# Optimization experiments

Measured on AMD Instinct MI355X. Metric: run time of the kernel, lower is better.

The kernel has to match this reference:

```python
import jax, jax.numpy as jnp
import numpy as np

LC, LQ, BATCH, D = 1024, 512, 64, 256

def setup_inputs() -> dict:
    key = jax.random.key(0)
    k1, k2, k3, k4, k5 = jax.random.split(key, 5)
    return {
        "C": jax.random.normal(k1, (LC, BATCH, D), dtype=jnp.float32),
        "Q": jax.random.normal(k2, (LQ, BATCH, D), dtype=jnp.float32),
        "w4C": jax.random.normal(k3, (D, 1), dtype=jnp.float32) * 0.05,
        "w4Q": jax.random.normal(k4, (D, 1), dtype=jnp.float32) * 0.05,
        "w4mlu": jax.random.normal(k5, (1, 1, D), dtype=jnp.float32) * 0.05,
        "bias": jnp.zeros((1,), dtype=jnp.float32),
    }

def reference(C, Q, w4C, w4Q, w4mlu, bias):
    # seq-major -> batch-major: (L, B, D) -> (B, L, D)
    C = jnp.transpose(C, (1, 0, 2))  # (B, Lc, D)
    Q = jnp.transpose(Q, (1, 0, 2))  # (B, Lq, D)
    # trilinear attention scores (dropout is identity in eval mode)
    sub0 = C @ w4C                                      # (B, Lc, 1)
    sub1 = jnp.transpose(Q @ w4Q, (0, 2, 1))            # (B, 1, Lq)
    sub2 = jnp.einsum('bcd,bqd->bcq', C * w4mlu, Q)     # (B, Lc, Lq)
    S = sub0 + sub1 + sub2 + bias                       # (B, Lc, Lq)
    S1 = jax.nn.softmax(S, axis=2)   # row softmax over query positions
    S2 = jax.nn.softmax(S, axis=1)   # col softmax over context positions
    A = jnp.einsum('bcq,bqd->bcd', S1, Q)               # (B, Lc, D)
    B_ = jnp.einsum('bck,bqk->bcq', S1, S2)             # S1 @ S2^T : (B, Lc, Lc)
    B_ = jnp.einsum('bce,bed->bcd', B_, C)              # (B, Lc, D)
    out = jnp.concatenate([C, A, C * A, C * B_], axis=2)  # (B, Lc, 4D)
    return jnp.transpose(out, (0, 2, 1))                  # (B, 4D, Lc)
```

## Files before the change

kernel.cpp:

```cpp
#include <hip/hip_runtime.h>

#define LCc 1024
#define LQq 512
#define BB  64
#define DDim 256

typedef __attribute__((ext_vector_type(8))) short bf16x8;
typedef __attribute__((ext_vector_type(4))) float f32x4;
typedef __attribute__((ext_vector_type(4))) unsigned short us4;
typedef __attribute__((ext_vector_type(8))) unsigned short us8;

static __device__ __forceinline__ unsigned short f2b(float f) {
  unsigned u = __builtin_bit_cast(unsigned, f);
  unsigned r = u + 0x7FFFu + ((u >> 16) & 1u);
  return (unsigned short)(r >> 16);
}
static __device__ __forceinline__ bf16x8 ldb8(const unsigned short* p) {
  return *(const bf16x8*)p;
}
static __device__ __forceinline__ f32x4 MFMA16(bf16x8 a, bf16x8 b, f32x4 c) {
  return __builtin_amdgcn_mfma_f32_16x16x32_bf16(a, b, c, 0, 0, 0);
}
static __device__ __forceinline__ void gload16(const unsigned short* g, unsigned short* l) {
  __builtin_amdgcn_global_load_lds(
      (const __attribute__((address_space(1))) unsigned int*)g,
      (__attribute__((address_space(3))) unsigned int*)l, 16, 0, 0);
}

__global__ __launch_bounds__(256, 4) void prep_CF(const float* __restrict__ C,
    const float* __restrict__ w4C, const float* __restrict__ w4mlu,
    unsigned short* __restrict__ Cw, unsigned short* __restrict__ CT,
    float* __restrict__ rowAdd) {
  __shared__ unsigned short tile[64][65];
  int c0 = blockIdx.x * 64, b = blockIdx.y;
  int t = threadIdx.x, r = t >> 2, g = t & 3;
  float rsum = 0.f;
  for (int dch = 0; dch < 4; dch++) {
    int d0 = dch * 64;
    const float* src = C + ((size_t)(c0 + r) * BB + b) * DDim + d0 + g * 16;
    unsigned short cwv[16];
    #pragma unroll
    for (int i = 0; i < 4; i++) {
      float4 v = ((const float4*)src)[i];
      float4 wm = *(const float4*)(w4mlu + d0 + g * 16 + i * 4);
      float4 wc = *(const float4*)(w4C + d0 + g * 16 + i * 4);
      rsum += v.x * wc.x + v.y * wc.y + v.z * wc.z + v.w * wc.w;
      cwv[i * 4 + 0] = f2b(v.x * wm.x);
      cwv[i * 4 + 1] = f2b(v.y * wm.y);
      cwv[i * 4 + 2] = f2b(v.z * wm.z);
      cwv[i * 4 + 3] = f2b(v.w * wm.w);
      tile[r][g * 16 + i * 4 + 0] = f2b(v.x);
      tile[r][g * 16 + i * 4 + 1] = f2b(v.y);
      tile[r][g * 16 + i * 4 + 2] = f2b(v.z);
      tile[r][g * 16 + i * 4 + 3] = f2b(v.w);
    }
    unsigned short* cwp = Cw + ((size_t)((b << 10) + c0 + r)) * DDim + d0 + g * 16;
    *(us8*)cwp = *(us8*)&cwv[0];
    *(us8*)(cwp + 8) = *(us8*)&cwv[8];
    __syncthreads();
    unsigned short* ctp = CT + ((size_t)((b << 8) + d0 + r)) * LCc + c0 + g * 16;
    us8 o0, o1;
    #pragma unroll
    for (int j = 0; j < 8; j++) { o0[j] = tile[g * 16 + j][r]; o1[j] = tile[g * 16 + 8 + j][r]; }
    *(us8*)ctp = o0;
    *(us8*)(ctp + 8) = o1;
    __syncthreads();
  }
  rsum += __shfl_xor(rsum, 1);
  rsum += __shfl_xor(rsum, 2);
  if (g == 0) rowAdd[((size_t)b << 10) + c0 + r] = rsum;
}

__global__ __launch_bounds__(256, 4) void prep_QF(const float* __restrict__ Q,
    const float* __restrict__ w4Q, const float* __restrict__ bias,
    unsigned short* __restrict__ Qb, unsigned short* __restrict__ QT,
    float* __restrict__ colAdd, float* __restrict__ colL) {
  __shared__ unsigned short tile[64][65];
  int q0 = blockIdx.x * 64, b = blockIdx.y;
  int t = threadIdx.x, r = t >> 2, g = t & 3;
  float rsum = 0.f;
  for (int dch = 0; dch < 4; dch++) {
    int d0 = dch * 64;
    const float* src = Q + ((size_t)(q0 + r) * BB + b) * DDim + d0 + g * 16;
    #pragma unroll
    for (int i = 0; i < 4; i++) {
      float4 v = ((const float4*)src)[i];
      float4 wq = *(const float4*)(w4Q + d0 + g * 16 + i * 4);
      rsum += v.x * wq.x + v.y * wq.y + v.z * wq.z + v.w * wq.w;
      tile[r][g * 16 + i * 4 + 0] = f2b(v.x);
      tile[r][g * 16 + i * 4 + 1] = f2b(v.y);
      tile[r][g * 16 + i * 4 + 2] = f2b(v.z);
      tile[r][g * 16 + i * 4 + 3] = f2b(v.w);
    }
    __syncthreads();
    unsigned short* qbp = Qb + ((size_t)((b << 9) + q0 + r)) * DDim + d0 + g * 16;
    us8 s0, s1;
    #pragma unroll
    for (int j = 0; j < 8; j++) { s0[j] = tile[r][g * 16 + j]; s1[j] = tile[r][g * 16 + 8 + j]; }
    *(us8*)qbp = s0;
    *(us8*)(qbp + 8) = s1;
    unsigned short* qtp = QT + ((size_t)((b << 8) + d0 + r)) * LQq + q0 + g * 16;
    us8 o0, o1;
    #pragma unroll
    for (int j = 0; j < 8; j++) { o0[j] = tile[g * 16 + j][r]; o1[j] = tile[g * 16 + 8 + j][r]; }
    *(us8*)qtp = o0;
    *(us8*)(qtp + 8) = o1;
    __syncthreads();
  }
  rsum += __shfl_xor(rsum, 1);
  rsum += __shfl_xor(rsum, 2);
  if (g == 0) {
    colAdd[((size_t)b << 9) + q0 + r] = rsum + bias[0];
    colL[((size_t)b << 9) + q0 + r] = 0.0f;
  }
}

__global__ __launch_bounds__(256, 3) void k_P(const unsigned short* __restrict__ Cw,
    const unsigned short* __restrict__ Qb, const float* __restrict__ rowAdd,
    const float* __restrict__ colAdd, unsigned short* __restrict__ Pt,
    float* __restrict__ rowL, float* __restrict__ colL) {
  int blk = blockIdx.x;
  int b = blk >> 4, ct = blk & 15;
  int t = threadIdx.x, w = t >> 6, lane = t & 63;
  int col = lane & 15, quad = lane >> 4;
  int c0w = ct * 64 + w * 16;
  __shared__ unsigned short tile[2][64][40];
  __shared__ float colAcc[LQq];
  for (int i = t; i < LQq; i += 256) colAcc[i] = 0.f;
  __syncthreads();

  bf16x8 afrag[8];
  const unsigned short* aPtr = Cw + ((size_t)((b << 10) + c0w + col)) * DDim + quad * 8;
  #pragma unroll
  for (int kk = 0; kk < 8; kk++) afrag[kk] = ldb8(aPtr + kk * 32);
  float rAddv[4];
  #pragma unroll
  for (int r = 0; r < 4; r++) rAddv[r] = rowAdd[((size_t)b << 10) + c0w + quad * 4 + r];
  float rowSum[4] = {0.f, 0.f, 0.f, 0.f};

  int cur = 0;
  for (int win = 0; win < 16; win++) {
    #pragma unroll
    for (int h = 0; h < 2; h++) {
      int q0 = win * 32 + h * 16;
      const unsigned short* bPtr = Qb + ((size_t)((b << 9) + q0 + col)) * DDim + quad * 8;
      f32x4 acc = {0.f, 0.f, 0.f, 0.f};
      #pragma unroll
      for (int kk = 0; kk < 8; kk++) acc = MFMA16(afrag[kk], ldb8(bPtr + kk * 32), acc);
      float cAdd = colAdd[((size_t)b << 9) + q0 + col];
      float csum = 0.f;
      #pragma unroll
      for (int r = 0; r < 4; r++) {
        float e = __expf(acc[r] + rAddv[r] + cAdd);
        rowSum[r] += e;
        csum += e;
        tile[cur][w * 16 + quad * 4 + r][h * 16 + col] = f2b(e);
      }
      csum += __shfl_xor(csum, 16);
      csum += __shfl_xor(csum, 32);
      if (lane < 16) atomicAdd(&colAcc[q0 + lane], csum);
    }
    __syncthreads();
    us8 frag = *(const us8*)&tile[cur][w * 16 + col][quad * 8];
    *(us8*)(Pt + (((size_t)(b * 64 + ct * 4 + w) * 16 + win) << 9) + lane * 8) = frag;
    cur ^= 1;
  }
  #pragma unroll
  for (int r = 0; r < 4; r++) {
    float s = rowSum[r];
    s += __shfl_xor(s, 1); s += __shfl_xor(s, 2);
    s += __shfl_xor(s, 4); s += __shfl_xor(s, 8);
    if (col == 0) rowL[((size_t)b << 10) + c0w + quad * 4 + r] = s;
  }
  __syncthreads();
  for (int i = t; i < LQq; i += 256) atomicAdd(&colL[((size_t)b << 9) + i], colAcc[i]);
}

__global__ __launch_bounds__(256, 4) void k_T(const unsigned short* __restrict__ Pt,
    const unsigned short* __restrict__ CT, const float* __restrict__ colL,
    unsigned short* __restrict__ TT) {
  int blk = blockIdx.x;
  int b = blk >> 4, qs = blk & 15;
  int t = threadIdx.x, w = t >> 6, lane = t & 63;
  int col = lane & 15, quad = lane >> 4;
  int dq = w * 64;
  int cbl = w & 1, jh = w >> 1;
  __shared__ unsigned short pT[32][40];

  f32x4 accT[2][4];
  #pragma unroll
  for (int mf = 0; mf < 2; mf++)
    #pragma unroll
    for (int nf = 0; nf < 4; nf++) accT[mf][nf] = (f32x4){0.f, 0.f, 0.f, 0.f};

  us8 frag = *(const us8*)(Pt + (((size_t)(b * 64 + 0 * 2 + cbl) * 16 + qs) << 9) + lane * 8);
  for (int cs = 0; cs < 32; cs++) {
    bf16x8 bf[4];
    #pragma unroll
    for (int nf = 0; nf < 4; nf++)
      bf[nf] = ldb8(CT + ((size_t)((b << 8) + dq + nf * 16 + col)) * LCc + cs * 32 + quad * 8);
    #pragma unroll
    for (int jj = 0; jj < 4; jj++) {
      int j = jh * 4 + jj;
      pT[quad * 8 + j][cbl * 16 + col] = (unsigned short)frag[j];
    }
    __syncthreads();
    bf16x8 pa[2];
    #pragma unroll
    for (int mf = 0; mf < 2; mf++) pa[mf] = *(const bf16x8*)&pT[mf * 16 + col][quad * 8];
    #pragma unroll
    for (int mf = 0; mf < 2; mf++)
      #pragma unroll
      for (int nf = 0; nf < 4; nf++) accT[mf][nf] = MFMA16(pa[mf], bf[nf], accT[mf][nf]);
    if (cs < 31)
      frag = *(const us8*)(Pt + (((size_t)(b * 64 + (cs + 1) * 2 + cbl) * 16 + qs) << 9) + lane * 8);
    __syncthreads();
  }
  float cInv[2][4];
  #pragma unroll
  for (int mf = 0; mf < 2; mf++)
    #pragma unroll
    for (int r = 0; r < 4; r++)
      cInv[mf][r] = 1.0f / colL[((size_t)b << 9) + qs * 32 + mf * 16 + quad * 4 + r];
  #pragma unroll
  for (int mf = 0; mf < 2; mf++)
    #pragma unroll
    for (int nf = 0; nf < 4; nf++) {
      us4 ov;
      #pragma unroll
      for (int r = 0; r < 4; r++) ov[r] = f2b(accT[mf][nf][r] * cInv[mf][r]);
      *(us4*)(TT + ((size_t)((b << 8) + dq + nf * 16 + col)) * LQq + qs * 32 + mf * 16 + quad * 4) = ov;
    }
}

__global__ __launch_bounds__(256, 2) void k_AB(const unsigned short* __restrict__ Pt,
    const unsigned short* __restrict__ QT, const unsigned short* __restrict__ TT,
    const float* __restrict__ rowL, const float* __restrict__ C,
    float* __restrict__ out) {
  int blk = blockIdx.x;
  int b = blk >> 4, ct = blk & 15;
  int t = threadIdx.x, w = t >> 6, lane = t & 63;
  int col = lane & 15, quad = lane >> 4;
  int dq = w * 64;
  __shared__ unsigned short sb[4][2][8][512];

  f32x4 accA[4][4], accB[4][4];
  #pragma unroll
  for (int mf = 0; mf < 4; mf++)
    #pragma unroll
    for (int nf = 0; nf < 4; nf++) {
      accA[mf][nf] = (f32x4){0.f, 0.f, 0.f, 0.f};
      accB[mf][nf] = (f32x4){0.f, 0.f, 0.f, 0.f};
    }

  #define STAGE(qs_, buf_)                                                              \
    {                                                                                   \
      int _q = (qs_) * 32 + quad * 8;                                                   \
      _Pragma("unroll")                                                                 \
      for (int nf = 0; nf < 4; nf++) {                                                  \
        size_t rowD = (size_t)((b << 8) + dq + nf * 16 + col);                          \
        gload16(QT + (rowD << 9) + _q, &sb[w][buf_][nf][0]);                            \
        gload16(TT + (rowD << 9) + _q, &sb[w][buf_][4 + nf][0]);                        \
      }                                                                                 \
    }

  bf16x8 pa[4], paN[4];
  #pragma unroll
  for (int mf = 0; mf < 4; mf++)
    pa[mf] = ldb8(Pt + (((size_t)(b * 64 + ct * 4 + mf) * 16 + 0) << 9) + lane * 8);
  STAGE(0, 0);
  __syncthreads();

  for (int qs = 0; qs < 16; qs++) {
    int bufr = qs & 1;
    if (qs < 15) {
      STAGE(qs + 1, bufr ^ 1);
      #pragma unroll
      for (int mf = 0; mf < 4; mf++)
        paN[mf] = ldb8(Pt + (((size_t)(b * 64 + ct * 4 + mf) * 16 + qs + 1) << 9) + lane * 8);
    }
    bf16x8 bq[4], bt[4];
    #pragma unroll
    for (int nf = 0; nf < 4; nf++) {
      bq[nf] = ldb8(&sb[w][bufr][nf][lane * 8]);
      bt[nf] = ldb8(&sb[w][bufr][4 + nf][lane * 8]);
    }
    #pragma unroll
    for (int mf = 0; mf < 4; mf++)
      #pragma unroll
      for (int nf = 0; nf < 4; nf++) {
        accA[mf][nf] = MFMA16(pa[mf], bq[nf], accA[mf][nf]);
        accB[mf][nf] = MFMA16(pa[mf], bt[nf], accB[mf][nf]);
      }
    if (qs < 15) {
      #pragma unroll
      for (int mf = 0; mf < 4; mf++) pa[mf] = paN[mf];
    }
    __syncthreads();
  }

  float rInv[4][4];
  #pragma unroll
  for (int mf = 0; mf < 4; mf++) {
    float4 rv = *(const float4*)(rowL + ((size_t)b << 10) + ct * 64 + mf * 16 + quad * 4);
    rInv[mf][0] = 1.0f / rv.x; rInv[mf][1] = 1.0f / rv.y;
    rInv[mf][2] = 1.0f / rv.z; rInv[mf][3] = 1.0f / rv.w;
  }
  size_t outB = (size_t)b << 20;
  #pragma unroll
  for (int mf = 0; mf < 4; mf++) {
    int cc = ct * 64 + mf * 16 + quad * 4;
    #pragma unroll
    for (int nf = 0; nf < 4; nf++) {
      int d = dq + nf * 16 + col;
      float4 vC, vA, vCA, vCB;
      #pragma unroll
      for (int r = 0; r < 4; r++) {
        float Cv = C[((size_t)(cc + r) * BB + b) * DDim + d];
        float Av = accA[mf][nf][r] * rInv[mf][r];
        float Bv = accB[mf][nf][r] * rInv[mf][r];
        ((float*)&vC)[r] = Cv;
        ((float*)&vA)[r] = Av;
        ((float*)&vCA)[r] = Cv * Av;
        ((float*)&vCB)[r] = Cv * Bv;
      }
      float* o0 = out + outB + (size_t)d * LCc + cc;
      *(float4*)(o0) = vC;
      *(float4*)(o0 + (size_t)DDim * LCc) = vA;
      *(float4*)(o0 + 2 * (size_t)DDim * LCc) = vCA;
      *(float4*)(o0 + 3 * (size_t)DDim * LCc) = vCB;
    }
  }
  #undef STAGE
}

extern "C" void kernel_launch(void* const* d_in, const int* in_sizes, int n_in,
                              void* d_out, int out_size, void* d_ws, size_t ws_size,
                              hipStream_t stream) {
  const float* C    = (const float*)d_in[0];
  const float* Q    = (const float*)d_in[1];
  const float* w4C  = (const float*)d_in[2];
  const float* w4Q  = (const float*)d_in[3];
  const float* w4mlu= (const float*)d_in[4];
  const float* bias = (const float*)d_in[5];
  float* out = (float*)d_out;
  char* ws = (char*)d_ws;

  unsigned short* Cw = (unsigned short*)(ws);
  unsigned short* CT = (unsigned short*)(ws + 33554432);
  unsigned short* Qb = (unsigned short*)(ws + 67108864);
  unsigned short* TT = Qb;
  unsigned short* QT = (unsigned short*)(ws + 83886080);
  unsigned short* Pt = (unsigned short*)(ws + 100663296);
  float* rowAdd = (float*)(ws + 167772160);
  float* colAdd = (float*)(ws + 168034304);
  float* rowL   = (float*)(ws + 168165376);
  float* colL   = (float*)(ws + 168427520);

  prep_CF<<<dim3(LCc / 64, BB), 256, 0, stream>>>(C, w4C, w4mlu, Cw, CT, rowAdd);
  prep_QF<<<dim3(LQq / 64, BB), 256, 0, stream>>>(Q, w4Q, bias, Qb, QT, colAdd, colL);
  k_P<<<BB * 16, 256, 0, stream>>>(Cw, Qb, rowAdd, colAdd, Pt, rowL, colL);
  k_T<<<BB * 16, 256, 0, stream>>>(Pt, CT, colL, TT);
  k_AB<<<BB * 16, 256, 0, stream>>>(Pt, QT, TT, rowL, C, out);
}
```

Baseline: 687.3 us.

## Merge prep kernels, remap blocks per XCD, double-buffer k_T LDS tile

Merges the two prep kernels into a single launch that branches on blockIdx.x to handle either C or Q tiles, saving one kernel launch and the tail gap between them. Remaps block indices in k_P, k_T and k_AB so that all blocks for a given batch land on the same XCD, which should improve L2 reuse of the per-batch operands. In k_T, the pT staging tile is double-buffered and the next Pt fragment is prefetched before the barrier, dropping one __syncthreads per iteration. The costs are extra LDS in k_T and a mapping that assumes round-robin dispatch of blocks across 8 XCDs.

```diff
diff --git a/kernel.cpp b/kernel.cpp
--- a/kernel.cpp
+++ b/kernel.cpp
@@ -27,91 +27,90 @@
       (__attribute__((address_space(3))) unsigned int*)l, 16, 0, 0);
 }
 
-__global__ __launch_bounds__(256, 4) void prep_CF(const float* __restrict__ C,
-    const float* __restrict__ w4C, const float* __restrict__ w4mlu,
+__global__ __launch_bounds__(256, 4) void prep_F(const float* __restrict__ C,
+    const float* __restrict__ Q, const float* __restrict__ w4C,
+    const float* __restrict__ w4Q, const float* __restrict__ w4mlu,
+    const float* __restrict__ bias,
     unsigned short* __restrict__ Cw, unsigned short* __restrict__ CT,
-    float* __restrict__ rowAdd) {
-  __shared__ unsigned short tile[64][65];
-  int c0 = blockIdx.x * 64, b = blockIdx.y;
-  int t = threadIdx.x, r = t >> 2, g = t & 3;
-  float rsum = 0.f;
-  for (int dch = 0; dch < 4; dch++) {
-    int d0 = dch * 64;
-    const float* src = C + ((size_t)(c0 + r) * BB + b) * DDim + d0 + g * 16;
-    unsigned short cwv[16];
-    #pragma unroll
-    for (int i = 0; i < 4; i++) {
-      float4 v = ((const float4*)src)[i];
-      float4 wm = *(const float4*)(w4mlu + d0 + g * 16 + i * 4);
-      float4 wc = *(const float4*)(w4C + d0 + g * 16 + i * 4);
-      rsum += v.x * wc.x + v.y * wc.y + v.z * wc.z + v.w * wc.w;
-      cwv[i * 4 + 0] = f2b(v.x * wm.x);
-      cwv[i * 4 + 1] = f2b(v.y * wm.y);
-      cwv[i * 4 + 2] = f2b(v.z * wm.z);
-      cwv[i * 4 + 3] = f2b(v.w * wm.w);
-      tile[r][g * 16 + i * 4 + 0] = f2b(v.x);
-      tile[r][g * 16 + i * 4 + 1] = f2b(v.y);
-      tile[r][g * 16 + i * 4 + 2] = f2b(v.z);
-      tile[r][g * 16 + i * 4 + 3] = f2b(v.w);
-    }
-    unsigned short* cwp = Cw + ((size_t)((b << 10) + c0 + r)) * DDim + d0 + g * 16;
-    *(us8*)cwp = *(us8*)&cwv[0];
-    *(us8*)(cwp + 8) = *(us8*)&cwv[8];
-    __syncthreads();
-    unsigned short* ctp = CT + ((size_t)((b << 8) + d0 + r)) * LCc + c0 + g * 16;
-    us8 o0, o1;
-    #pragma unroll
-    for (int j = 0; j < 8; j++) { o0[j] = tile[g * 16 + j][r]; o1[j] = tile[g * 16 + 8 + j][r]; }
-    *(us8*)ctp = o0;
-    *(us8*)(ctp + 8) = o1;
-    __syncthreads();
-  }
-  rsum += __shfl_xor(rsum, 1);
-  rsum += __shfl_xor(rsum, 2);
-  if (g == 0) rowAdd[((size_t)b << 10) + c0 + r] = rsum;
-}
-
-__global__ __launch_bounds__(256, 4) void prep_QF(const float* __restrict__ Q,
-    const float* __restrict__ w4Q, const float* __restrict__ bias,
+    float* __restrict__ rowAdd,
     unsigned short* __restrict__ Qb, unsigned short* __restrict__ QT,
     float* __restrict__ colAdd, float* __restrict__ colL) {
   __shared__ unsigned short tile[64][65];
-  int q0 = blockIdx.x * 64, b = blockIdx.y;
+  int b = blockIdx.y;
   int t = threadIdx.x, r = t >> 2, g = t & 3;
   float rsum = 0.f;
-  for (int dch = 0; dch < 4; dch++) {
-    int d0 = dch * 64;
-    const float* src = Q + ((size_t)(q0 + r) * BB + b) * DDim + d0 + g * 16;
-    #pragma unroll
-    for (int i = 0; i < 4; i++) {
-      float4 v = ((const float4*)src)[i];
-      float4 wq = *(const float4*)(w4Q + d0 + g * 16 + i * 4);
-      rsum += v.x * wq.x + v.y * wq.y + v.z * wq.z + v.w * wq.w;
-      tile[r][g * 16 + i * 4 + 0] = f2b(v.x);
-      tile[r][g * 16 + i * 4 + 1] = f2b(v.y);
-      tile[r][g * 16 + i * 4 + 2] = f2b(v.z);
-      tile[r][g * 16 + i * 4 + 3] = f2b(v.w);
-    }
-    __syncthreads();
-    unsigned short* qbp = Qb + ((size_t)((b << 9) + q0 + r)) * DDim + d0 + g * 16;
-    us8 s0, s1;
-    #pragma unroll
-    for (int j = 0; j < 8; j++) { s0[j] = tile[r][g * 16 + j]; s1[j] = tile[r][g * 16 + 8 + j]; }
-    *(us8*)qbp = s0;
-    *(us8*)(qbp + 8) = s1;
-    unsigned short* qtp = QT + ((size_t)((b << 8) + d0 + r)) * LQq + q0 + g * 16;
-    us8 o0, o1;
-    #pragma unroll
-    for (int j = 0; j < 8; j++) { o0[j] = tile[g * 16 + j][r]; o1[j] = tile[g * 16 + 8 + j][r]; }
-    *(us8*)qtp = o0;
-    *(us8*)(qtp + 8) = o1;
-    __syncthreads();
-  }
-  rsum += __shfl_xor(rsum, 1);
-  rsum += __shfl_xor(rsum, 2);
-  if (g == 0) {
-    colAdd[((size_t)b << 9) + q0 + r] = rsum + bias[0];
-    colL[((size_t)b << 9) + q0 + r] = 0.0f;
+  if (blockIdx.x < 16) {
+    int c0 = blockIdx.x * 64;
+    for (int dch = 0; dch < 4; dch++) {
+      int d0 = dch * 64;
+      const float* src = C + ((size_t)(c0 + r) * BB + b) * DDim + d0 + g * 16;
+      unsigned short cwv[16];
+      #pragma unroll
+      for (int i = 0; i < 4; i++) {
+        float4 v = ((const float4*)src)[i];
+        float4 wm = *(const float4*)(w4mlu + d0 + g * 16 + i * 4);
+        float4 wc = *(const float4*)(w4C + d0 + g * 16 + i * 4);
+        rsum += v.x * wc.x + v.y * wc.y + v.z * wc.z + v.w * wc.w;
+        cwv[i * 4 + 0] = f2b(v.x * wm.x);
+        cwv[i * 4 + 1] = f2b(v.y * wm.y);
+        cwv[i * 4 + 2] = f2b(v.z * wm.z);
+        cwv[i * 4 + 3] = f2b(v.w * wm.w);
+        tile[r][g * 16 + i * 4 + 0] = f2b(v.x);
+        tile[r][g * 16 + i * 4 + 1] = f2b(v.y);
+        tile[r][g * 16 + i * 4 + 2] = f2b(v.z);
+        tile[r][g * 16 + i * 4 + 3] = f2b(v.w);
+      }
+      unsigned short* cwp = Cw + ((size_t)((b << 10) + c0 + r)) * DDim + d0 + g * 16;
+      *(us8*)cwp = *(us8*)&cwv[0];
+      *(us8*)(cwp + 8) = *(us8*)&cwv[8];
+      __syncthreads();
+      unsigned short* ctp = CT + ((size_t)((b << 8) + d0 + r)) * LCc + c0 + g * 16;
+      us8 o0, o1;
+      #pragma unroll
+      for (int j = 0; j < 8; j++) { o0[j] = tile[g * 16 + j][r]; o1[j] = tile[g * 16 + 8 + j][r]; }
+      *(us8*)ctp = o0;
+      *(us8*)(ctp + 8) = o1;
+      __syncthreads();
+    }
+    rsum += __shfl_xor(rsum, 1);
+    rsum += __shfl_xor(rsum, 2);
+    if (g == 0) rowAdd[((size_t)b << 10) + c0 + r] = rsum;
+  } else {
+    int q0 = (blockIdx.x - 16) * 64;
+    for (int dch = 0; dch < 4; dch++) {
+      int d0 = dch * 64;
+      const float* src = Q + ((size_t)(q0 + r) * BB + b) * DDim + d0 + g * 16;
+      #pragma unroll
+      for (int i = 0; i < 4; i++) {
+        float4 v = ((const float4*)src)[i];
+        float4 wq = *(const float4*)(w4Q + d0 + g * 16 + i * 4);
+        rsum += v.x * wq.x + v.y * wq.y + v.z * wq.z + v.w * wq.w;
+        tile[r][g * 16 + i * 4 + 0] = f2b(v.x);
+        tile[r][g * 16 + i * 4 + 1] = f2b(v.y);
+        tile[r][g * 16 + i * 4 + 2] = f2b(v.z);
+        tile[r][g * 16 + i * 4 + 3] = f2b(v.w);
+      }
+      __syncthreads();
+      unsigned short* qbp = Qb + ((size_t)((b << 9) + q0 + r)) * DDim + d0 + g * 16;
+      us8 s0, s1;
+      #pragma unroll
+      for (int j = 0; j < 8; j++) { s0[j] = tile[r][g * 16 + j]; s1[j] = tile[r][g * 16 + 8 + j]; }
+      *(us8*)qbp = s0;
+      *(us8*)(qbp + 8) = s1;
+      unsigned short* qtp = QT + ((size_t)((b << 8) + d0 + r)) * LQq + q0 + g * 16;
+      us8 o0, o1;
+      #pragma unroll
+      for (int j = 0; j < 8; j++) { o0[j] = tile[g * 16 + j][r]; o1[j] = tile[g * 16 + 8 + j][r]; }
+      *(us8*)qtp = o0;
+      *(us8*)(qtp + 8) = o1;
+      __syncthreads();
+    }
+    rsum += __shfl_xor(rsum, 1);
+    rsum += __shfl_xor(rsum, 2);
+    if (g == 0) {
+      colAdd[((size_t)b << 9) + q0 + r] = rsum + bias[0];
+      colL[((size_t)b << 9) + q0 + r] = 0.0f;
+    }
   }
 }
 
@@ -119,8 +118,9 @@
     const unsigned short* __restrict__ Qb, const float* __restrict__ rowAdd,
     const float* __restrict__ colAdd, unsigned short* __restrict__ Pt,
     float* __restrict__ rowL, float* __restrict__ colL) {
-  int blk = blockIdx.x;
-  int b = blk >> 4, ct = blk & 15;
+  int idx = blockIdx.x;
+  int xcd = idx & 7, jj = idx >> 3;
+  int b = xcd * 8 + (jj >> 4), ct = jj & 15;
   int t = threadIdx.x, w = t >> 6, lane = t & 63;
   int col = lane & 15, quad = lane >> 4;
   int c0w = ct * 64 + w * 16;
@@ -179,13 +179,14 @@
 __global__ __launch_bounds__(256, 4) void k_T(const unsigned short* __restrict__ Pt,
     const unsigned short* __restrict__ CT, const float* __restrict__ colL,
     unsigned short* __restrict__ TT) {
-  int blk = blockIdx.x;
-  int b = blk >> 4, qs = blk & 15;
+  int idx = blockIdx.x;
+  int xcd = idx & 7, jj = idx >> 3;
+  int b = xcd * 8 + (jj >> 4), qs = jj & 15;
   int t = threadIdx.x, w = t >> 6, lane = t & 63;
   int col = lane & 15, quad = lane >> 4;
   int dq = w * 64;
   int cbl = w & 1, jh = w >> 1;
-  __shared__ unsigned short pT[32][40];
+  __shared__ unsigned short pT[2][32][40];
 
   f32x4 accT[2][4];
   #pragma unroll
@@ -200,21 +201,22 @@
     for (int nf = 0; nf < 4; nf++)
       bf[nf] = ldb8(CT + ((size_t)((b << 8) + dq + nf * 16 + col)) * LCc + cs * 32 + quad * 8);
     #pragma unroll
-    for (int jj = 0; jj < 4; jj++) {
-      int j = jh * 4 + jj;
-      pT[quad * 8 + j][cbl * 16 + col] = (unsigned short)frag[j];
-    }
+    for (int j2 = 0; j2 < 4; j2++) {
+      int j = jh * 4 + j2;
+      pT[cs & 1][quad * 8 + j][cbl * 16 + col] = (unsigned short)frag[j];
+    }
+    us8 fragN;
+    if (cs < 31)
+      fragN = *(const us8*)(Pt + (((size_t)(b * 64 + (cs + 1) * 2 + cbl) * 16 + qs) << 9) + lane * 8);
     __syncthreads();
     bf16x8 pa[2];
     #pragma unroll
-    for (int mf = 0; mf < 2; mf++) pa[mf] = *(const bf16x8*)&pT[mf * 16 + col][quad * 8];
+    for (int mf = 0; mf < 2; mf++) pa[mf] = *(const bf16x8*)&pT[cs & 1][mf * 16 + col][quad * 8];
     #pragma unroll
     for (int mf = 0; mf < 2; mf++)
       #pragma unroll
       for (int nf = 0; nf < 4; nf++) accT[mf][nf] = MFMA16(pa[mf], bf[nf], accT[mf][nf]);
-    if (cs < 31)
-      frag = *(const us8*)(Pt + (((size_t)(b * 64 + (cs + 1) * 2 + cbl) * 16 + qs) << 9) + lane * 8);
-    __syncthreads();
+    frag = fragN;
   }
   float cInv[2][4];
   #pragma unroll
@@ -237,8 +239,9 @@
     const unsigned short* __restrict__ QT, const unsigned short* __restrict__ TT,
     const float* __restrict__ rowL, const float* __restrict__ C,
     float* __restrict__ out) {
-  int blk = blockIdx.x;
-  int b = blk >> 4, ct = blk & 15;
+  int idx = blockIdx.x;
+  int xcd = idx & 7, jj = idx >> 3;
+  int b = xcd * 8 + (jj >> 4), ct = jj & 15;
   int t = threadIdx.x, w = t >> 6, lane = t & 63;
   int col = lane & 15, quad = lane >> 4;
   int dq = w * 64;
@@ -357,8 +360,8 @@
   float* rowL   = (float*)(ws + 168165376);
   float* colL   = (float*)(ws + 168427520);
 
-  prep_CF<<<dim3(LCc / 64, BB), 256, 0, stream>>>(C, w4C, w4mlu, Cw, CT, rowAdd);
-  prep_QF<<<dim3(LQq / 64, BB), 256, 0, stream>>>(Q, w4Q, bias, Qb, QT, colAdd, colL);
+  prep_F<<<dim3(24, BB), 256, 0, stream>>>(C, Q, w4C, w4Q, w4mlu, bias,
+                                           Cw, CT, rowAdd, Qb, QT, colAdd, colL);
   k_P<<<BB * 16, 256, 0, stream>>>(Cw, Qb, rowAdd, colAdd, Pt, rowL, colL);
   k_T<<<BB * 16, 256, 0, stream>>>(Pt, CT, colL, TT);
   k_AB<<<BB * 16, 256, 0, stream>>>(Pt, QT, TT, rowL, C, out);
```

New measurement: 681.4 us. No clear change (-0.9%).
